# Kernel tuning notes

Measured on AMD Instinct MI355X. Metric: run time of the kernel, lower is better.

The kernel has to match this reference:

```python
import jax, jax.numpy as jnp
import numpy as np

B, S, D = 4, 2048, 1024
H, DK, DV = 16, 64, 64
FF = 4096
EPS = 1e-6


def _ln(x, g, b):
    mu = jnp.mean(x, axis=-1, keepdims=True)
    var = jnp.mean((x - mu) ** 2, axis=-1, keepdims=True)
    return (x - mu) * jax.lax.rsqrt(var + EPS) * g + b


def setup_inputs() -> dict:
    key = jax.random.key(0)
    ks = jax.random.split(key, 12)
    sd = 0.02
    return {
        "src": jax.random.normal(ks[0], (B, S, D), jnp.float32),
        "attn_mask": jnp.zeros((B, S, S), jnp.bool_),
        "Wq": jax.random.normal(ks[1], (D, H * DK), jnp.float32) * sd,
        "bq": jnp.zeros((H * DK,), jnp.float32),
        "Wk": jax.random.normal(ks[2], (D, H * DK), jnp.float32) * sd,
        "bk": jnp.zeros((H * DK,), jnp.float32),
        "Wv": jax.random.normal(ks[3], (D, H * DV), jnp.float32) * sd,
        "bv": jnp.zeros((H * DV,), jnp.float32),
        "Wo": jax.random.normal(ks[4], (D, D), jnp.float32) * sd,
        "bo": jnp.zeros((D,), jnp.float32),
        "ln1_g": jnp.ones((D,), jnp.float32),
        "ln1_b": jnp.zeros((D,), jnp.float32),
        "W1": jax.random.normal(ks[5], (D, FF), jnp.float32) * sd,
        "b1": jnp.zeros((FF,), jnp.float32),
        "W2": jax.random.normal(ks[6], (FF, D), jnp.float32) * sd,
        "b2": jnp.zeros((D,), jnp.float32),
        "ln2_g": jnp.ones((D,), jnp.float32),
        "ln2_b": jnp.zeros((D,), jnp.float32),
    }


def reference(src, attn_mask, Wq, bq, Wk, bk, Wv, bv, Wo, bo,
              ln1_g, ln1_b, W1, b1, W2, b2, ln2_g, ln2_b):
    # QKV projections, split heads: [B,S,H*dk] -> [B,H,S,dk]
    q = (src @ Wq + bq).reshape(B, S, H, DK).transpose(0, 2, 1, 3)
    k = (src @ Wk + bk).reshape(B, S, H, DK).transpose(0, 2, 1, 3)
    v = (src @ Wv + bv).reshape(B, S, H, DV).transpose(0, 2, 1, 3)

    scale = 1.0 / (DK ** 0.5)
    scores = jnp.einsum("bhqd,bhkd->bhqk", q, k) * scale
    scores = jnp.where(attn_mask[:, None, :, :], -1e9, scores)
    attn = jax.nn.softmax(scores, axis=-1)  # dropout = identity (eval)
    ctx = jnp.einsum("bhqk,bhkd->bhqd", attn, v)
    ctx = ctx.transpose(0, 2, 1, 3).reshape(B, S, D)

    att_out = ctx @ Wo + bo  # dropout = identity (eval)
    x = _ln(src + att_out, ln1_g, ln1_b)

    h = jax.nn.relu(x @ W1 + b1)  # dropout = identity (eval)
    ffn_out = h @ W2 + b2
    return _ln(ffn_out + x, ln2_g, ln2_b)
```

## Files before the change

kernel.cpp:

```cpp
#include <hip/hip_runtime.h>
#include <stdint.h>

#define BB 4
#define SS 2048
#define DMODEL 1024
#define NH 16
#define FF 4096
#define MROWS (BB*SS)

typedef __bf16 bf16x8 __attribute__((ext_vector_type(8)));
typedef __bf16 bf16x2t __attribute__((ext_vector_type(2)));
typedef float f32x4 __attribute__((ext_vector_type(4)));
typedef float f32x16 __attribute__((ext_vector_type(16)));
typedef unsigned uintx4 __attribute__((ext_vector_type(4)));

__device__ __forceinline__ unsigned short f2b(float f) {
  unsigned u = __float_as_uint(f);
  unsigned r = (u + 0x7FFFu + ((u >> 16) & 1u)) >> 16;
  return (unsigned short)r;
}

__device__ __forceinline__ unsigned pack2bf(float a, float b) {
  bf16x2t v = {(__bf16)a, (__bf16)b};
  return __builtin_bit_cast(unsigned, v);
}

__device__ __forceinline__ void pls32(unsigned& x, unsigned& y) {
#if defined(__has_builtin) && __has_builtin(__builtin_amdgcn_permlane32_swap)
  auto r = __builtin_amdgcn_permlane32_swap(x, y, 0, 0);
  x = (unsigned)r[0];
  y = (unsigned)r[1];
#else
  const unsigned sx = (unsigned)__shfl_xor((int)x, 32, 64);
  const unsigned sy = (unsigned)__shfl_xor((int)y, 32, 64);
  const bool hi = ((threadIdx.x >> 5) & 1) != 0;
  const unsigned nx = hi ? sy : x;
  const unsigned ny = hi ? y : sx;
  x = nx; y = ny;
#endif
}

__device__ __forceinline__ void gload_lds16(const void* g, void* l) {
  __builtin_amdgcn_global_load_lds(
      (const __attribute__((address_space(1))) void*)g,
      (__attribute__((address_space(3))) void*)l, 16, 0, 0);
}

__device__ __forceinline__ bf16x8 frag_rot(const unsigned short* base, int row, int kElem) {
  const int cb = kElem * 2;
  const unsigned off = (unsigned)(row * 128 + ((((cb >> 4) + row) & 7) << 4) + (cb & 15));
  return *reinterpret_cast<const bf16x8*>(reinterpret_cast<const char*>(base) + off);
}

__global__ __launch_bounds__(256) void f32_to_bf16_k(const float* __restrict__ in,
                                                     unsigned short* __restrict__ out, int n8) {
  const int i = blockIdx.x * 256 + threadIdx.x;
  if (i >= n8) return;
  const float4* p = reinterpret_cast<const float4*>(in) + (size_t)i * 2;
  const float4 a = p[0], c = p[1];
  uint4 o;
  o.x = (unsigned)f2b(a.x) | ((unsigned)f2b(a.y) << 16);
  o.y = (unsigned)f2b(a.z) | ((unsigned)f2b(a.w) << 16);
  o.z = (unsigned)f2b(c.x) | ((unsigned)f2b(c.y) << 16);
  o.w = (unsigned)f2b(c.z) | ((unsigned)f2b(c.w) << 16);
  reinterpret_cast<uint4*>(out)[i] = o;
}

__global__ __launch_bounds__(256) void transpose_convert_k(const float* __restrict__ in,
                                                           unsigned short* __restrict__ out,
                                                           int R, int C) {
  __shared__ float tile[32][33];
  const int c0 = blockIdx.x * 32, r0 = blockIdx.y * 32;
  const int tx = threadIdx.x, ty = threadIdx.y;
  #pragma unroll
  for (int i = 0; i < 4; ++i)
    tile[ty + i * 8][tx] = in[(size_t)(r0 + ty + i * 8) * C + c0 + tx];
  __syncthreads();
  #pragma unroll
  for (int i = 0; i < 4; ++i)
    out[(size_t)(c0 + ty + i * 8) * R + r0 + tx] = f2b(tile[tx][ty + i * 8]);
}

__global__ __launch_bounds__(256) void v_transpose_k(const unsigned short* __restrict__ Vb,
                                                     unsigned short* __restrict__ Vt) {
  __shared__ unsigned short tile[32][33];
  const int bh = blockIdx.z, b = bh >> 4, h = bh & 15;
  const int s0 = blockIdx.x * 32, d0 = blockIdx.y * 32;
  const int tx = threadIdx.x, ty = threadIdx.y;
  #pragma unroll
  for (int i = 0; i < 4; ++i)
    tile[ty + i * 8][tx] = Vb[(size_t)(b * SS + s0 + ty + i * 8) * DMODEL + h * 64 + d0 + tx];
  __syncthreads();
  #pragma unroll
  for (int i = 0; i < 4; ++i)
    Vt[(size_t)(bh * 64 + d0 + ty + i * 8) * SS + s0 + tx] = tile[tx][ty + i * 8];
}

__global__ __launch_bounds__(256) void mask_pack_k(const unsigned char* __restrict__ mask,
                                                   unsigned long long* __restrict__ mbits, int total) {
  const int idx = blockIdx.x * 256 + threadIdx.x;
  if (idx >= total) return;
  const uint4* p = reinterpret_cast<const uint4*>(mask) + (size_t)idx * 4;
  unsigned long long bits = 0ull;
  #pragma unroll
  for (int q = 0; q < 4; ++q) {
    uint4 v = p[q];
    unsigned wds[4] = {v.x, v.y, v.z, v.w};
    #pragma unroll
    for (int j = 0; j < 4; ++j)
      #pragma unroll
      for (int by = 0; by < 4; ++by)
        if ((wds[j] >> (by * 8)) & 0xFFu) bits |= 1ull << (q * 16 + j * 4 + by);
  }
  mbits[idx] = bits;
}

template <int EPI>
__global__ __launch_bounds__(256, 2) void gemm2_k(const unsigned short* __restrict__ A,
                                                  const unsigned short* __restrict__ Bt,
                                                  const float* __restrict__ bias_a,
                                                  const float* __restrict__ bias_b,
                                                  const float* __restrict__ bias_c,
                                                  void* __restrict__ Cout, int N, int K) {
  __shared__ __align__(16) unsigned short As[2][128 * 64];
  __shared__ __align__(16) unsigned short Bs[2][128 * 64];
  const int t = threadIdx.x;
  const int lane = t & 63, w = t >> 6;
  const int wr = w >> 1, wc = w & 1;
  const int lr = lane & 15, lg = lane >> 4;

  const int nwg = gridDim.x;
  const int q8 = nwg >> 3;
  const int wg = (blockIdx.x & 7) * q8 + (blockIdx.x >> 3);
  const int mb = wg & 63, nb = wg >> 6;
  const int m0 = mb * 128, n0 = nb * 128;

  const int srow = t >> 3;
  const int g = ((t & 7) - srow) & 7;
  const char* Asrc = reinterpret_cast<const char*>(A) + ((size_t)(m0 + srow) * K + g * 8) * 2;
  const char* Bsrc = reinterpret_cast<const char*>(Bt) + ((size_t)(n0 + srow) * K + g * 8) * 2;
  const size_t rstep = (size_t)32 * K * 2;
  char* AsB[2] = {reinterpret_cast<char*>(As[0]) + w * 1024, reinterpret_cast<char*>(As[1]) + w * 1024};
  char* BsB[2] = {reinterpret_cast<char*>(Bs[0]) + w * 1024, reinterpret_cast<char*>(Bs[1]) + w * 1024};

  auto stage = [&](int buf, int kt) {
    const char* ak = Asrc + (size_t)kt * 128;
    const char* bk = Bsrc + (size_t)kt * 128;
    #pragma unroll
    for (int c = 0; c < 4; ++c) {
      gload_lds16(ak + c * rstep, AsB[buf] + c * 4096);
      gload_lds16(bk + c * rstep, BsB[buf] + c * 4096);
    }
  };

  f32x4 acc[4][4] = {};
  const int nt = K >> 6;

  stage(0, 0);
  stage(1, 1);
  asm volatile("s_waitcnt vmcnt(8)" ::: "memory");
  __builtin_amdgcn_s_barrier();

  int cur = 0;
  for (int kt = 0; kt < nt; ++kt) {
    bf16x8 af[2][4], bfr[2][4];
    #pragma unroll
    for (int kk = 0; kk < 2; ++kk) {
      #pragma unroll
      for (int m = 0; m < 4; ++m)
        af[kk][m] = frag_rot(As[cur], wr * 64 + m * 16 + lr, kk * 32 + lg * 8);
      #pragma unroll
      for (int n = 0; n < 4; ++n)
        bfr[kk][n] = frag_rot(Bs[cur], wc * 64 + n * 16 + lr, kk * 32 + lg * 8);
    }
    __builtin_amdgcn_s_setprio(1);
    #pragma unroll
    for (int m = 0; m < 4; ++m)
      #pragma unroll
      for (int n = 0; n < 4; ++n)
        acc[m][n] = __builtin_amdgcn_mfma_f32_16x16x32_bf16(af[0][m], bfr[0][n], acc[m][n], 0, 0, 0);
    __builtin_amdgcn_s_setprio(0);

    asm volatile("s_waitcnt lgkmcnt(0)" ::: "memory");
    __builtin_amdgcn_s_barrier();
    if (kt + 2 < nt) {
      stage(cur, kt + 2);
      asm volatile("s_waitcnt vmcnt(8)" ::: "memory");
    } else {
      asm volatile("s_waitcnt vmcnt(0)" ::: "memory");
    }
    __builtin_amdgcn_s_barrier();
    __builtin_amdgcn_sched_barrier(0);

    __builtin_amdgcn_s_setprio(1);
    #pragma unroll
    for (int m = 0; m < 4; ++m)
      #pragma unroll
      for (int n = 0; n < 4; ++n)
        acc[m][n] = __builtin_amdgcn_mfma_f32_16x16x32_bf16(af[1][m], bfr[1][n], acc[m][n], 0, 0, 0);
    __builtin_amdgcn_s_setprio(0);
    cur ^= 1;
  }

  const int ccol0 = wc * 64;
  if constexpr (EPI == 3) {
    const int g3 = n0 >> 10;
    const float* bias = (g3 == 0) ? bias_a : (g3 == 1) ? bias_b : bias_c;
    unsigned short* Og = reinterpret_cast<unsigned short*>(Cout) + (size_t)g3 * MROWS * DMODEL;
    const int ncol0 = (n0 & 1023) + ccol0;
    float bv[4];
    #pragma unroll
    for (int n = 0; n < 4; ++n) bv[n] = bias[ncol0 + n * 16 + lr];
    #pragma unroll
    for (int m = 0; m < 4; ++m)
      #pragma unroll
      for (int n = 0; n < 4; ++n)
        #pragma unroll
        for (int i = 0; i < 4; ++i) {
          const float v = acc[m][n][i] + bv[n];
          const size_t row = (size_t)(m0 + wr * 64 + m * 16 + lg * 4 + i);
          Og[row * DMODEL + (ncol0 + n * 16 + lr)] = f2b(v);
        }
  } else {
    float bv[4];
    #pragma unroll
    for (int n = 0; n < 4; ++n) bv[n] = bias_a[n0 + ccol0 + n * 16 + lr];
    #pragma unroll
    for (int m = 0; m < 4; ++m)
      #pragma unroll
      for (int n = 0; n < 4; ++n)
        #pragma unroll
        for (int i = 0; i < 4; ++i) {
          float v = acc[m][n][i] + bv[n];
          if (EPI == 1) v = fmaxf(v, 0.0f);
          const size_t row = (size_t)(m0 + wr * 64 + m * 16 + lg * 4 + i);
          const size_t col = (size_t)(n0 + ccol0 + n * 16 + lr);
          if (EPI == 2) reinterpret_cast<float*>(Cout)[row * N + col] = v;
          else          reinterpret_cast<unsigned short*>(Cout)[row * N + col] = f2b(v);
        }
  }
}

__global__ __launch_bounds__(256) void attn4_k(const unsigned short* __restrict__ Qb,
                                               const unsigned short* __restrict__ Kb,
                                               const unsigned short* __restrict__ Vt,
                                               const unsigned long long* __restrict__ mbits,
                                               unsigned short* __restrict__ ctx) {
  __shared__ __align__(16) unsigned short smem[16384];
  unsigned short* KsC = smem;
  unsigned short* KsN = smem + 4096;
  unsigned short* VsC = smem + 8192;
  unsigned short* VsN = smem + 12288;

  const int t = threadIdx.x;
  const int lane = t & 63, w = t >> 6;
  const int lo = lane & 31, hi = lane >> 5;

  const int flat = blockIdx.x;
  const int bid = (flat & 7) * 128 + (flat >> 3);
  const int bh = bid >> 4, qb = bid & 15;
  const int b = bh >> 4, h = bh & 15;
  const int q0 = qb * 128 + w * 32;

  bf16x8 qf[4];
  {
    const unsigned short* qp = Qb + (size_t)(b * SS + q0 + lo) * DMODEL + h * 64 + hi * 8;
    #pragma unroll
    for (int ds = 0; ds < 4; ++ds) qf[ds] = *reinterpret_cast<const bf16x8*>(qp + ds * 16);
  }

  f32x16 ao0 = {}, ao1 = {};
  float lrun = 0.0f;
  const float C = 0.18033688011112042f;

  const int srow = t >> 3;
  const int gsw = ((t & 7) - srow) & 7;
  const char* Ksrc = reinterpret_cast<const char*>(Kb) +
                     ((size_t)(b * SS + srow) * DMODEL + h * 64 + gsw * 8) * 2;
  const char* Vsrc = reinterpret_cast<const char*>(Vt) +
                     ((size_t)(bh * 64 + srow) * SS + gsw * 8) * 2;
  const unsigned wdo = (unsigned)(w * 1024);

  auto stage = [&](int kv, unsigned short* Kbuf, unsigned short* Vbuf) {
    const char* ks0 = Ksrc + (size_t)kv * (64 * DMODEL * 2);
    const char* vs0 = Vsrc + (size_t)kv * 128;
    char* kd = reinterpret_cast<char*>(Kbuf) + wdo;
    char* vd = reinterpret_cast<char*>(Vbuf) + wdo;
    gload_lds16(ks0, kd);
    gload_lds16(ks0 + (size_t)32 * DMODEL * 2, kd + 4096);
    gload_lds16(vs0, vd);
    gload_lds16(vs0 + (size_t)32 * SS * 2, vd + 4096);
  };

  stage(0, KsC, VsC);
  asm volatile("s_waitcnt vmcnt(0)" ::: "memory");
  __syncthreads();

  for (int kv = 0; kv < SS / 64; ++kv) {
    if (kv + 1 < SS / 64) stage(kv + 1, KsN, VsN);

    const unsigned long long mb =
        mbits[(size_t)(b * SS + q0 + lo) * (SS / 64) + kv];

    f32x16 st0 = {}, st1 = {};
    __builtin_amdgcn_s_setprio(1);
    #pragma unroll
    for (int ds = 0; ds < 4; ++ds) {
      const int kcol = ds * 16 + hi * 8;
      const bf16x8 k0 = frag_rot(KsC, lo, kcol);
      const bf16x8 k1 = frag_rot(KsC, 32 + lo, kcol);
      st0 = __builtin_amdgcn_mfma_f32_32x32x16_bf16(k0, qf[ds], st0, 0, 0, 0);
      st1 = __builtin_amdgcn_mfma_f32_32x32x16_bf16(k1, qf[ds], st1, 0, 0, 0);
    }
    __builtin_amdgcn_s_setprio(0);

    if (__any(mb != 0ull)) {
      #pragma unroll
      for (int r = 0; r < 16; ++r) {
        const int k = (r & 3) + 8 * (r >> 2) + 4 * hi;
        if ((mb >> k) & 1ull) st0[r] = -8.0e9f;
        if ((mb >> (k + 32)) & 1ull) st1[r] = -8.0e9f;
      }
    }

    float ls = 0.0f;
    #pragma unroll
    for (int r = 0; r < 16; ++r) {
      st0[r] = exp2f(st0[r] * C);
      st1[r] = exp2f(st1[r] * C);
      ls += st0[r] + st1[r];
    }
    ls += __shfl_xor(ls, 32, 64);
    lrun += ls;

    unsigned pw[16];
    #define PACK8(SV, KB)                                            \
      {                                                              \
        unsigned c0 = pack2bf(SV[0], SV[1]);                         \
        unsigned c1 = pack2bf(SV[2], SV[3]);                         \
        unsigned c2 = pack2bf(SV[4], SV[5]);                         \
        unsigned c3 = pack2bf(SV[6], SV[7]);                         \
        unsigned c4 = pack2bf(SV[8], SV[9]);                         \
        unsigned c5 = pack2bf(SV[10], SV[11]);                       \
        unsigned c6 = pack2bf(SV[12], SV[13]);                       \
        unsigned c7 = pack2bf(SV[14], SV[15]);                       \
        pls32(c0, c2); pls32(c1, c3); pls32(c4, c6); pls32(c5, c7);  \
        pw[(KB) + 0] = c0; pw[(KB) + 1] = c1;                        \
        pw[(KB) + 2] = c2; pw[(KB) + 3] = c3;                        \
        pw[(KB) + 4] = c4; pw[(KB) + 5] = c5;                        \
        pw[(KB) + 6] = c6; pw[(KB) + 7] = c7;                        \
      }
    PACK8(st0, 0)
    PACK8(st1, 8)
    #undef PACK8

    __builtin_amdgcn_s_setprio(1);
    #pragma unroll
    for (int ks = 0; ks < 4; ++ks) {
      const uintx4 pv = {pw[ks * 4 + 0], pw[ks * 4 + 1], pw[ks * 4 + 2], pw[ks * 4 + 3]};
      const bf16x8 pb = __builtin_bit_cast(bf16x8, pv);
      const int scol = ks * 16 + hi * 8;
      ao0 = __builtin_amdgcn_mfma_f32_32x32x16_bf16(frag_rot(VsC, lo, scol), pb, ao0, 0, 0, 0);
      ao1 = __builtin_amdgcn_mfma_f32_32x32x16_bf16(frag_rot(VsC, 32 + lo, scol), pb, ao1, 0, 0, 0);
    }
    __builtin_amdgcn_s_setprio(0);

    asm volatile("s_waitcnt vmcnt(0)" ::: "memory");
    __syncthreads();
    unsigned short* tk = KsC; KsC = KsN; KsN = tk;
    unsigned short* tv = VsC; VsC = VsN; VsN = tv;
  }

  const float inv = 1.0f / lrun;
  unsigned short* Ob = smem + w * 2048;
  #pragma unroll
  for (int dt = 0; dt < 2; ++dt) {
    #pragma unroll
    for (int r = 0; r < 16; ++r) {
      const int d = dt * 32 + (r & 3) + 8 * (r >> 2) + 4 * hi;
      const float v = (dt ? ao1[r] : ao0[r]) * inv;
      const unsigned off = (unsigned)((lo * 128 + d * 2) ^ ((lo & 7) << 4));
      *reinterpret_cast<unsigned short*>(reinterpret_cast<char*>(Ob) + off) = f2b(v);
    }
  }
  __syncthreads();
  const int rr = lane >> 1, xh = (lane & 1) * 64;
  char* crow_g = reinterpret_cast<char*>(ctx) +
                 ((size_t)(b * SS + q0 + rr) * DMODEL + h * 64) * 2;
  #pragma unroll
  for (int c = 0; c < 4; ++c) {
    const unsigned off = (unsigned)((rr * 128 + xh + c * 16) ^ ((rr & 7) << 4));
    const uint4 vv = *reinterpret_cast<const uint4*>(reinterpret_cast<const char*>(Ob) + off);
    *reinterpret_cast<uint4*>(crow_g + xh + c * 16) = vv;
  }
}

__global__ __launch_bounds__(256) void ln_k(const float* __restrict__ a,
                                            const float* __restrict__ res,
                                            const float* __restrict__ g,
                                            const float* __restrict__ be,
                                            float* __restrict__ of,
                                            unsigned short* __restrict__ ob) {
  const int row = blockIdx.x, t = threadIdx.x;
  float4 v = reinterpret_cast<const float4*>(a + (size_t)row * DMODEL)[t];
  const float4 r = reinterpret_cast<const float4*>(res + (size_t)row * DMODEL)[t];
  v.x += r.x; v.y += r.y; v.z += r.z; v.w += r.w;
  float s = v.x + v.y + v.z + v.w;
  float ss = v.x * v.x + v.y * v.y + v.z * v.z + v.w * v.w;
  #pragma unroll
  for (int off = 1; off < 64; off <<= 1) {
    s += __shfl_xor(s, off, 64);
    ss += __shfl_xor(ss, off, 64);
  }
  __shared__ float red[8];
  const int wv = t >> 6;
  if ((t & 63) == 0) { red[wv] = s; red[4 + wv] = ss; }
  __syncthreads();
  s = red[0] + red[1] + red[2] + red[3];
  ss = red[4] + red[5] + red[6] + red[7];
  const float mu = s * (1.0f / DMODEL);
  const float rs = rsqrtf(ss * (1.0f / DMODEL) - mu * mu + 1e-6f);
  const float4 gg = reinterpret_cast<const float4*>(g)[t];
  const float4 bb = reinterpret_cast<const float4*>(be)[t];
  float4 o;
  o.x = (v.x - mu) * rs * gg.x + bb.x;
  o.y = (v.y - mu) * rs * gg.y + bb.y;
  o.z = (v.z - mu) * rs * gg.z + bb.z;
  o.w = (v.w - mu) * rs * gg.w + bb.w;
  if (of) reinterpret_cast<float4*>(of + (size_t)row * DMODEL)[t] = o;
  if (ob) {
    ushort4 u;
    u.x = f2b(o.x); u.y = f2b(o.y); u.z = f2b(o.z); u.w = f2b(o.w);
    reinterpret_cast<ushort4*>(ob + (size_t)row * DMODEL)[t] = u;
  }
}

extern "C" void kernel_launch(void* const* d_in, const int* in_sizes, int n_in,
                              void* d_out, int out_size, void* d_ws, size_t ws_size,
                              hipStream_t stream) {
  const float* src = (const float*)d_in[0];
  const unsigned char* mask = (const unsigned char*)d_in[1];
  const float* Wq = (const float*)d_in[2];
  const float* bq = (const float*)d_in[3];
  const float* Wk = (const float*)d_in[4];
  const float* bk = (const float*)d_in[5];
  const float* Wv = (const float*)d_in[6];
  const float* bv = (const float*)d_in[7];
  const float* Wo = (const float*)d_in[8];
  const float* bo = (const float*)d_in[9];
  const float* ln1_g = (const float*)d_in[10];
  const float* ln1_b = (const float*)d_in[11];
  const float* W1 = (const float*)d_in[12];
  const float* b1 = (const float*)d_in[13];
  const float* W2 = (const float*)d_in[14];
  const float* b2 = (const float*)d_in[15];
  const float* ln2_g = (const float*)d_in[16];
  const float* ln2_b = (const float*)d_in[17];

  char* ws = (char*)d_ws;
  size_t off = 0;
  auto alloc = [&](size_t bytes) {
    char* p = ws + off;
    off += (bytes + 255) & ~(size_t)255;
    return p;
  };
  unsigned short* srcb = (unsigned short*)alloc((size_t)MROWS * DMODEL * 2);
  unsigned short* WqT  = (unsigned short*)alloc((size_t)DMODEL * DMODEL * 2);
  unsigned short* WkT  = (unsigned short*)alloc((size_t)DMODEL * DMODEL * 2);
  unsigned short* WvT  = (unsigned short*)alloc((size_t)DMODEL * DMODEL * 2);
  unsigned short* WoT  = (unsigned short*)alloc((size_t)DMODEL * DMODEL * 2);
  unsigned short* W1T  = (unsigned short*)alloc((size_t)FF * DMODEL * 2);
  unsigned short* W2T  = (unsigned short*)alloc((size_t)DMODEL * FF * 2);
  unsigned short* Qb   = (unsigned short*)alloc((size_t)MROWS * DMODEL * 2);
  unsigned short* Kb   = (unsigned short*)alloc((size_t)MROWS * DMODEL * 2);
  unsigned short* Vb   = (unsigned short*)alloc((size_t)MROWS * DMODEL * 2);
  unsigned short* Vt   = (unsigned short*)alloc((size_t)MROWS * DMODEL * 2);
  unsigned short* ctx  = (unsigned short*)alloc((size_t)MROWS * DMODEL * 2);
  float*          xf   = (float*)alloc((size_t)MROWS * DMODEL * 4);
  unsigned short* xb   = (unsigned short*)alloc((size_t)MROWS * DMODEL * 2);
  unsigned short* hb   = (unsigned short*)alloc((size_t)MROWS * FF * 2);
  unsigned long long* mbits = (unsigned long long*)alloc((size_t)BB * SS * (SS / 64) * 8);
  float* outf = (float*)d_out;
  (void)Kb; (void)Vb;

  f32_to_bf16_k<<<(MROWS * DMODEL / 8 + 255) / 256, 256, 0, stream>>>(src, srcb, MROWS * DMODEL / 8);
  dim3 tb(32, 8);
  transpose_convert_k<<<dim3(32, 32), tb, 0, stream>>>(Wq, WqT, DMODEL, DMODEL);
  transpose_convert_k<<<dim3(32, 32), tb, 0, stream>>>(Wk, WkT, DMODEL, DMODEL);
  transpose_convert_k<<<dim3(32, 32), tb, 0, stream>>>(Wv, WvT, DMODEL, DMODEL);
  transpose_convert_k<<<dim3(32, 32), tb, 0, stream>>>(Wo, WoT, DMODEL, DMODEL);
  transpose_convert_k<<<dim3(FF / 32, 32), tb, 0, stream>>>(W1, W1T, DMODEL, FF);
  transpose_convert_k<<<dim3(32, FF / 32), tb, 0, stream>>>(W2, W2T, FF, DMODEL);
  mask_pack_k<<<(BB * SS * (SS / 64) + 255) / 256, 256, 0, stream>>>(mask, mbits, BB * SS * (SS / 64));

  gemm2_k<3><<<dim3(64 * 24), 256, 0, stream>>>(srcb, WqT, bq, bk, bv, Qb, 3072, DMODEL);

  v_transpose_k<<<dim3(SS / 32, 2, BB * NH), tb, 0, stream>>>(Vb, Vt);

  attn4_k<<<dim3((SS / 128) * BB * NH), 256, 0, stream>>>(Qb, Kb, Vt, mbits, ctx);

  gemm2_k<2><<<dim3(64 * 8), 256, 0, stream>>>(ctx, WoT, bo, nullptr, nullptr, outf, DMODEL, DMODEL);

  ln_k<<<MROWS, 256, 0, stream>>>(outf, src, ln1_g, ln1_b, xf, xb);

  gemm2_k<1><<<dim3(64 * 32), 256, 0, stream>>>(xb, W1T, b1, nullptr, nullptr, hb, FF, DMODEL);
  gemm2_k<2><<<dim3(64 * 8), 256, 0, stream>>>(hb, W2T, b2, nullptr, nullptr, outf, DMODEL, FF);

  ln_k<<<MROWS, 256, 0, stream>>>(outf, xf, ln2_g, ln2_b, outf, nullptr);
}
```

Measured before the change: 512.3 us.

## Double attention query rows per wave, prescale Q in projection, swap LDS swizzle

```diff
diff --git a/kernel.cpp b/kernel.cpp
--- a/kernel.cpp
+++ b/kernel.cpp
@@ -46,6 +46,11 @@
       (__attribute__((address_space(3))) void*)l, 16, 0, 0);
 }
 
+__device__ __forceinline__ bf16x8 lds_frag(const unsigned short* base, int row, int k) {
+  unsigned off = (unsigned)((row * 128 + k * 2) ^ ((row & 7) << 4));
+  return *reinterpret_cast<const bf16x8*>(reinterpret_cast<const char*>(base) + off);
+}
+
 __device__ __forceinline__ bf16x8 frag_rot(const unsigned short* base, int row, int kElem) {
   const int cb = kElem * 2;
   const unsigned off = (unsigned)(row * 128 + ((((cb >> 4) + row) & 7) << 4) + (cb & 15));
@@ -66,6 +71,26 @@
   reinterpret_cast<uint4*>(out)[i] = o;
 }
 
+__global__ __launch_bounds__(256) void transpose_convert4_k(
+    const float* __restrict__ i0, const float* __restrict__ i1,
+    const float* __restrict__ i2, const float* __restrict__ i3,
+    unsigned short* __restrict__ o0, unsigned short* __restrict__ o1,
+    unsigned short* __restrict__ o2, unsigned short* __restrict__ o3) {
+  __shared__ float tile[32][33];
+  const int z = blockIdx.z;
+  const float* in = (z == 0) ? i0 : (z == 1) ? i1 : (z == 2) ? i2 : i3;
+  unsigned short* out = (z == 0) ? o0 : (z == 1) ? o1 : (z == 2) ? o2 : o3;
+  const int c0 = blockIdx.x * 32, r0 = blockIdx.y * 32;
+  const int tx = threadIdx.x, ty = threadIdx.y;
+  #pragma unroll
+  for (int i = 0; i < 4; ++i)
+    tile[ty + i * 8][tx] = in[(size_t)(r0 + ty + i * 8) * 1024 + c0 + tx];
+  __syncthreads();
+  #pragma unroll
+  for (int i = 0; i < 4; ++i)
+    out[(size_t)(c0 + ty + i * 8) * 1024 + r0 + tx] = f2b(tile[tx][ty + i * 8]);
+}
+
 __global__ __launch_bounds__(256) void transpose_convert_k(const float* __restrict__ in,
                                                            unsigned short* __restrict__ out,
                                                            int R, int C) {
@@ -115,6 +140,7 @@
   mbits[idx] = bits;
 }
 
+#define CQ 0.18033688011112042f
 template <int EPI>
 __global__ __launch_bounds__(256, 2) void gemm2_k(const unsigned short* __restrict__ A,
                                                   const unsigned short* __restrict__ Bt,
@@ -136,9 +162,9 @@
   const int m0 = mb * 128, n0 = nb * 128;
 
   const int srow = t >> 3;
-  const int g = ((t & 7) - srow) & 7;
-  const char* Asrc = reinterpret_cast<const char*>(A) + ((size_t)(m0 + srow) * K + g * 8) * 2;
-  const char* Bsrc = reinterpret_cast<const char*>(Bt) + ((size_t)(n0 + srow) * K + g * 8) * 2;
+  const unsigned cxor = (unsigned)(((t & 7) * 16) ^ (((t >> 3) & 7) << 4));
+  const char* Asrc = reinterpret_cast<const char*>(A) + ((size_t)(m0 + srow) * K) * 2 + cxor;
+  const char* Bsrc = reinterpret_cast<const char*>(Bt) + ((size_t)(n0 + srow) * K) * 2 + cxor;
   const size_t rstep = (size_t)32 * K * 2;
   char* AsB[2] = {reinterpret_cast<char*>(As[0]) + w * 1024, reinterpret_cast<char*>(As[1]) + w * 1024};
   char* BsB[2] = {reinterpret_cast<char*>(Bs[0]) + w * 1024, reinterpret_cast<char*>(Bs[1]) + w * 1024};
@@ -168,10 +194,10 @@
     for (int kk = 0; kk < 2; ++kk) {
       #pragma unroll
       for (int m = 0; m < 4; ++m)
-        af[kk][m] = frag_rot(As[cur], wr * 64 + m * 16 + lr, kk * 32 + lg * 8);
+        af[kk][m] = lds_frag(As[cur], wr * 64 + m * 16 + lr, kk * 32 + lg * 8);
       #pragma unroll
       for (int n = 0; n < 4; ++n)
-        bfr[kk][n] = frag_rot(Bs[cur], wc * 64 + n * 16 + lr, kk * 32 + lg * 8);
+        bfr[kk][n] = lds_frag(Bs[cur], wc * 64 + n * 16 + lr, kk * 32 + lg * 8);
     }
     __builtin_amdgcn_s_setprio(1);
     #pragma unroll
@@ -206,6 +232,7 @@
   if constexpr (EPI == 3) {
     const int g3 = n0 >> 10;
     const float* bias = (g3 == 0) ? bias_a : (g3 == 1) ? bias_b : bias_c;
+    const float scl = (g3 == 0) ? CQ : 1.0f;
     unsigned short* Og = reinterpret_cast<unsigned short*>(Cout) + (size_t)g3 * MROWS * DMODEL;
     const int ncol0 = (n0 & 1023) + ccol0;
     float bv[4];
@@ -217,7 +244,7 @@
       for (int n = 0; n < 4; ++n)
         #pragma unroll
         for (int i = 0; i < 4; ++i) {
-          const float v = acc[m][n][i] + bv[n];
+          const float v = (acc[m][n][i] + bv[n]) * scl;
           const size_t row = (size_t)(m0 + wr * 64 + m * 16 + lg * 4 + i);
           Og[row * DMODEL + (ncol0 + n * 16 + lr)] = f2b(v);
         }
@@ -241,7 +268,7 @@
   }
 }
 
-__global__ __launch_bounds__(256) void attn4_k(const unsigned short* __restrict__ Qb,
+__global__ __launch_bounds__(256) void attn7_k(const unsigned short* __restrict__ Qb,
                                                const unsigned short* __restrict__ Kb,
                                                const unsigned short* __restrict__ Vt,
                                                const unsigned long long* __restrict__ mbits,
@@ -257,21 +284,24 @@
   const int lo = lane & 31, hi = lane >> 5;
 
   const int flat = blockIdx.x;
-  const int bid = (flat & 7) * 128 + (flat >> 3);
-  const int bh = bid >> 4, qb = bid & 15;
+  const int bid = (flat & 7) * 64 + (flat >> 3);
+  const int bh = bid >> 3, qb = bid & 7;
   const int b = bh >> 4, h = bh & 15;
-  const int q0 = qb * 128 + w * 32;
-
-  bf16x8 qf[4];
+  const int q0 = qb * 256 + w * 64;
+
+  bf16x8 qfA[4], qfB[4];
   {
-    const unsigned short* qp = Qb + (size_t)(b * SS + q0 + lo) * DMODEL + h * 64 + hi * 8;
-    #pragma unroll
-    for (int ds = 0; ds < 4; ++ds) qf[ds] = *reinterpret_cast<const bf16x8*>(qp + ds * 16);
-  }
-
-  f32x16 ao0 = {}, ao1 = {};
-  float lrun = 0.0f;
-  const float C = 0.18033688011112042f;
+    const unsigned short* qpA = Qb + (size_t)(b * SS + q0 + lo) * DMODEL + h * 64 + hi * 8;
+    const unsigned short* qpB = qpA + (size_t)32 * DMODEL;
+    #pragma unroll
+    for (int ds = 0; ds < 4; ++ds) {
+      qfA[ds] = *reinterpret_cast<const bf16x8*>(qpA + ds * 16);
+      qfB[ds] = *reinterpret_cast<const bf16x8*>(qpB + ds * 16);
+    }
+  }
+
+  f32x16 aoA0 = {}, aoA1 = {}, aoB0 = {}, aoB1 = {};
+  float lrA = 0.0f, lrB = 0.0f;
 
   const int srow = t >> 3;
   const int gsw = ((t & 7) - srow) & 7;
@@ -292,76 +322,95 @@
     gload_lds16(vs0 + (size_t)32 * SS * 2, vd + 4096);
   };
 
+  const unsigned long long* mrA = mbits + (size_t)(b * SS + q0 + lo) * (SS / 64);
+  const unsigned long long* mrB = mrA + (size_t)32 * (SS / 64);
+
   stage(0, KsC, VsC);
   asm volatile("s_waitcnt vmcnt(0)" ::: "memory");
   __syncthreads();
 
+  #define SMPACK(ST0, ST1, MB, LRUN, PW)                                        \
+    {                                                                           \
+      if (__any((MB) != 0ull)) {                                                \
+        _Pragma("unroll")                                                       \
+        for (int r = 0; r < 16; ++r) {                                          \
+          const int k = (r & 3) + 8 * (r >> 2) + 4 * hi;                        \
+          if (((MB) >> k) & 1ull) ST0[r] = -20.0f;                              \
+          if (((MB) >> (k + 32)) & 1ull) ST1[r] = -20.0f;                       \
+        }                                                                       \
+      }                                                                         \
+      float ps[16];                                                             \
+      _Pragma("unroll")                                                         \
+      for (int r = 0; r < 16; ++r) {                                            \
+        ST0[r] = exp2f(ST0[r]);                                                 \
+        ST1[r] = exp2f(ST1[r]);                                                 \
+        ps[r] = ST0[r] + ST1[r];                                                \
+      }                                                                         \
+      _Pragma("unroll")                                                         \
+      for (int r = 0; r < 8; ++r) ps[r] += ps[r + 8];                           \
+      _Pragma("unroll")                                                         \
+      for (int r = 0; r < 4; ++r) ps[r] += ps[r + 4];                           \
+      float ls = (ps[0] + ps[1]) + (ps[2] + ps[3]);                             \
+      ls += __shfl_xor(ls, 32, 64);                                             \
+      LRUN += ls;                                                               \
+      {                                                                         \
+        unsigned c0 = pack2bf(ST0[0], ST0[1]),  c1 = pack2bf(ST0[2], ST0[3]);   \
+        unsigned c2 = pack2bf(ST0[4], ST0[5]),  c3 = pack2bf(ST0[6], ST0[7]);   \
+        unsigned c4 = pack2bf(ST0[8], ST0[9]),  c5 = pack2bf(ST0[10], ST0[11]); \
+        unsigned c6 = pack2bf(ST0[12], ST0[13]), c7 = pack2bf(ST0[14], ST0[15]);\
+        pls32(c0, c2); pls32(c1, c3); pls32(c4, c6); pls32(c5, c7);             \
+        PW[0] = c0; PW[1] = c1; PW[2] = c2; PW[3] = c3;                         \
+        PW[4] = c4; PW[5] = c5; PW[6] = c6; PW[7] = c7;                         \
+      }                                                                         \
+      {                                                                         \
+        unsigned c0 = pack2bf(ST1[0], ST1[1]),  c1 = pack2bf(ST1[2], ST1[3]);   \
+        unsigned c2 = pack2bf(ST1[4], ST1[5]),  c3 = pack2bf(ST1[6], ST1[7]);   \
+        unsigned c4 = pack2bf(ST1[8], ST1[9]),  c5 = pack2bf(ST1[10], ST1[11]); \
+        unsigned c6 = pack2bf(ST1[12], ST1[13]), c7 = pack2bf(ST1[14], ST1[15]);\
+        pls32(c0, c2); pls32(c1, c3); pls32(c4, c6); pls32(c5, c7);             \
+        PW[8] = c0;  PW[9] = c1;  PW[10] = c2; PW[11] = c3;                     \
+        PW[12] = c4; PW[13] = c5; PW[14] = c6; PW[15] = c7;                     \
+      }                                                                         \
+    }
+
   for (int kv = 0; kv < SS / 64; ++kv) {
     if (kv + 1 < SS / 64) stage(kv + 1, KsN, VsN);
 
-    const unsigned long long mb =
-        mbits[(size_t)(b * SS + q0 + lo) * (SS / 64) + kv];
-
-    f32x16 st0 = {}, st1 = {};
+    const unsigned long long mbA = mrA[kv];
+    const unsigned long long mbB = mrB[kv];
+
+    f32x16 sA0 = {}, sA1 = {}, sB0 = {}, sB1 = {};
     __builtin_amdgcn_s_setprio(1);
     #pragma unroll
     for (int ds = 0; ds < 4; ++ds) {
       const int kcol = ds * 16 + hi * 8;
       const bf16x8 k0 = frag_rot(KsC, lo, kcol);
       const bf16x8 k1 = frag_rot(KsC, 32 + lo, kcol);
-      st0 = __builtin_amdgcn_mfma_f32_32x32x16_bf16(k0, qf[ds], st0, 0, 0, 0);
-      st1 = __builtin_amdgcn_mfma_f32_32x32x16_bf16(k1, qf[ds], st1, 0, 0, 0);
+      sA0 = __builtin_amdgcn_mfma_f32_32x32x16_bf16(k0, qfA[ds], sA0, 0, 0, 0);
+      sA1 = __builtin_amdgcn_mfma_f32_32x32x16_bf16(k1, qfA[ds], sA1, 0, 0, 0);
+      sB0 = __builtin_amdgcn_mfma_f32_32x32x16_bf16(k0, qfB[ds], sB0, 0, 0, 0);
+      sB1 = __builtin_amdgcn_mfma_f32_32x32x16_bf16(k1, qfB[ds], sB1, 0, 0, 0);
     }
     __builtin_amdgcn_s_setprio(0);
 
-    if (__any(mb != 0ull)) {
-      #pragma unroll
-      for (int r = 0; r < 16; ++r) {
-        const int k = (r & 3) + 8 * (r >> 2) + 4 * hi;
-        if ((mb >> k) & 1ull) st0[r] = -8.0e9f;
-        if ((mb >> (k + 32)) & 1ull) st1[r] = -8.0e9f;
-      }
-    }
-
-    float ls = 0.0f;
-    #pragma unroll
-    for (int r = 0; r < 16; ++r) {
-      st0[r] = exp2f(st0[r] * C);
-      st1[r] = exp2f(st1[r] * C);
-      ls += st0[r] + st1[r];
-    }
-    ls += __shfl_xor(ls, 32, 64);
-    lrun += ls;
-
-    unsigned pw[16];
-    #define PACK8(SV, KB)                                            \
-      {                                                              \
-        unsigned c0 = pack2bf(SV[0], SV[1]);                         \
-        unsigned c1 = pack2bf(SV[2], SV[3]);                         \
-        unsigned c2 = pack2bf(SV[4], SV[5]);                         \
-        unsigned c3 = pack2bf(SV[6], SV[7]);                         \
-        unsigned c4 = pack2bf(SV[8], SV[9]);                         \
-        unsigned c5 = pack2bf(SV[10], SV[11]);                       \
-        unsigned c6 = pack2bf(SV[12], SV[13]);                       \
-        unsigned c7 = pack2bf(SV[14], SV[15]);                       \
-        pls32(c0, c2); pls32(c1, c3); pls32(c4, c6); pls32(c5, c7);  \
-        pw[(KB) + 0] = c0; pw[(KB) + 1] = c1;                        \
-        pw[(KB) + 2] = c2; pw[(KB) + 3] = c3;                        \
-        pw[(KB) + 4] = c4; pw[(KB) + 5] = c5;                        \
-        pw[(KB) + 6] = c6; pw[(KB) + 7] = c7;                        \
-      }
-    PACK8(st0, 0)
-    PACK8(st1, 8)
-    #undef PACK8
+    unsigned pwA[16], pwB[16];
+    SMPACK(sA0, sA1, mbA, lrA, pwA)
+    SMPACK(sB0, sB1, mbB, lrB, pwB)
 
     __builtin_amdgcn_s_setprio(1);
     #pragma unroll
     for (int ks = 0; ks < 4; ++ks) {
-      const uintx4 pv = {pw[ks * 4 + 0], pw[ks * 4 + 1], pw[ks * 4 + 2], pw[ks * 4 + 3]};
-      const bf16x8 pb = __builtin_bit_cast(bf16x8, pv);
       const int scol = ks * 16 + hi * 8;
-      ao0 = __builtin_amdgcn_mfma_f32_32x32x16_bf16(frag_rot(VsC, lo, scol), pb, ao0, 0, 0, 0);
-      ao1 = __builtin_amdgcn_mfma_f32_32x32x16_bf16(frag_rot(VsC, 32 + lo, scol), pb, ao1, 0, 0, 0);
+      const bf16x8 v0 = frag_rot(VsC, lo, scol);
+      const bf16x8 v1 = frag_rot(VsC, 32 + lo, scol);
+      const uintx4 pa = {pwA[ks * 4 + 0], pwA[ks * 4 + 1], pwA[ks * 4 + 2], pwA[ks * 4 + 3]};
+      const uintx4 pb = {pwB[ks * 4 + 0], pwB[ks * 4 + 1], pwB[ks * 4 + 2], pwB[ks * 4 + 3]};
+      const bf16x8 pA = __builtin_bit_cast(bf16x8, pa);
+      const bf16x8 pB = __builtin_bit_cast(bf16x8, pb);
+      aoA0 = __builtin_amdgcn_mfma_f32_32x32x16_bf16(v0, pA, aoA0, 0, 0, 0);
+      aoA1 = __builtin_amdgcn_mfma_f32_32x32x16_bf16(v1, pA, aoA1, 0, 0, 0);
+      aoB0 = __builtin_amdgcn_mfma_f32_32x32x16_bf16(v0, pB, aoB0, 0, 0, 0);
+      aoB1 = __builtin_amdgcn_mfma_f32_32x32x16_bf16(v1, pB, aoB1, 0, 0, 0);
     }
     __builtin_amdgcn_s_setprio(0);
 
@@ -370,29 +419,37 @@
     unsigned short* tk = KsC; KsC = KsN; KsN = tk;
     unsigned short* tv = VsC; VsC = VsN; VsN = tv;
   }
-
-  const float inv = 1.0f / lrun;
+  #undef SMPACK
+
   unsigned short* Ob = smem + w * 2048;
-  #pragma unroll
-  for (int dt = 0; dt < 2; ++dt) {
-    #pragma unroll
-    for (int r = 0; r < 16; ++r) {
-      const int d = dt * 32 + (r & 3) + 8 * (r >> 2) + 4 * hi;
-      const float v = (dt ? ao1[r] : ao0[r]) * inv;
-      const unsigned off = (unsigned)((lo * 128 + d * 2) ^ ((lo & 7) << 4));
-      *reinterpret_cast<unsigned short*>(reinterpret_cast<char*>(Ob) + off) = f2b(v);
-    }
-  }
-  __syncthreads();
   const int rr = lane >> 1, xh = (lane & 1) * 64;
-  char* crow_g = reinterpret_cast<char*>(ctx) +
-                 ((size_t)(b * SS + q0 + rr) * DMODEL + h * 64) * 2;
-  #pragma unroll
-  for (int c = 0; c < 4; ++c) {
-    const unsigned off = (unsigned)((rr * 128 + xh + c * 16) ^ ((rr & 7) << 4));
-    const uint4 vv = *reinterpret_cast<const uint4*>(reinterpret_cast<const char*>(Ob) + off);
-    *reinterpret_cast<uint4*>(crow_g + xh + c * 16) = vv;
-  }
+  #define EPIGRP(AO0, AO1, LRUN, QOFF)                                          \
+    {                                                                           \
+      const float inv = 1.0f / (LRUN);                                          \
+      _Pragma("unroll")                                                         \
+      for (int dt = 0; dt < 2; ++dt) {                                          \
+        _Pragma("unroll")                                                       \
+        for (int r = 0; r < 16; ++r) {                                          \
+          const int d = dt * 32 + (r & 3) + 8 * (r >> 2) + 4 * hi;              \
+          const float v = (dt ? (AO1)[r] : (AO0)[r]) * inv;                     \
+          const unsigned off = (unsigned)((lo * 128 + d * 2) ^ ((lo & 7) << 4));\
+          *reinterpret_cast<unsigned short*>(reinterpret_cast<char*>(Ob) + off) = f2b(v); \
+        }                                                                       \
+      }                                                                         \
+      asm volatile("s_waitcnt lgkmcnt(0)" ::: "memory");                        \
+      char* crow_g = reinterpret_cast<char*>(ctx) +                             \
+                     ((size_t)(b * SS + q0 + (QOFF) + rr) * DMODEL + h * 64) * 2; \
+      _Pragma("unroll")                                                         \
+      for (int c = 0; c < 4; ++c) {                                             \
+        const unsigned off = (unsigned)((rr * 128 + xh + c * 16) ^ ((rr & 7) << 4)); \
+        const uint4 vv = *reinterpret_cast<const uint4*>(reinterpret_cast<const char*>(Ob) + off); \
+        *reinterpret_cast<uint4*>(crow_g + xh + c * 16) = vv;                   \
+      }                                                                         \
+      asm volatile("s_waitcnt lgkmcnt(0)" ::: "memory");                        \
+    }
+  EPIGRP(aoA0, aoA1, lrA, 0)
+  EPIGRP(aoB0, aoB1, lrB, 32)
+  #undef EPIGRP
 }
 
 __global__ __launch_bounds__(256) void ln_k(const float* __restrict__ a,
@@ -485,10 +542,7 @@
 
   f32_to_bf16_k<<<(MROWS * DMODEL / 8 + 255) / 256, 256, 0, stream>>>(src, srcb, MROWS * DMODEL / 8);
   dim3 tb(32, 8);
-  transpose_convert_k<<<dim3(32, 32), tb, 0, stream>>>(Wq, WqT, DMODEL, DMODEL);
-  transpose_convert_k<<<dim3(32, 32), tb, 0, stream>>>(Wk, WkT, DMODEL, DMODEL);
-  transpose_convert_k<<<dim3(32, 32), tb, 0, stream>>>(Wv, WvT, DMODEL, DMODEL);
-  transpose_convert_k<<<dim3(32, 32), tb, 0, stream>>>(Wo, WoT, DMODEL, DMODEL);
+  transpose_convert4_k<<<dim3(32, 32, 4), tb, 0, stream>>>(Wq, Wk, Wv, Wo, WqT, WkT, WvT, WoT);
   transpose_convert_k<<<dim3(FF / 32, 32), tb, 0, stream>>>(W1, W1T, DMODEL, FF);
   transpose_convert_k<<<dim3(32, FF / 32), tb, 0, stream>>>(W2, W2T, FF, DMODEL);
   mask_pack_k<<<(BB * SS * (SS / 64) + 255) / 256, 256, 0, stream>>>(mask, mbits, BB * SS * (SS / 64));
@@ -497,7 +551,7 @@
 
   v_transpose_k<<<dim3(SS / 32, 2, BB * NH), tb, 0, stream>>>(Vb, Vt);
 
-  attn4_k<<<dim3((SS / 128) * BB * NH), 256, 0, stream>>>(Qb, Kb, Vt, mbits, ctx);
+  attn7_k<<<dim3((SS / 256) * BB * NH), 256, 0, stream>>>(Qb, Kb, Vt, mbits, ctx);
 
   gemm2_k<2><<<dim3(64 * 8), 256, 0, stream>>>(ctx, WoT, bo, nullptr, nullptr, outf, DMODEL, DMODEL);
 
```

New measurement: 521.2 us. Within noise of the previous version (+1.7%).
